# Performance work log

Hardware: AMD Instinct MI355X
Metric: run time of the kernel (lower is better)

The kernel has to match this reference:

```python
import jax, jax.numpy as jnp
import numpy as np


def setup_inputs() -> dict:
    key = jax.random.key(0)
    x = jax.random.normal(key, (4, 5, 256, 32, 32), dtype=jnp.float32)
    return {"x": x, "beta": 1}


def reference(x, beta):
    # x: [B, L, D, H, W] -> [B, L, H, W, D] -> [B, L, N, D], N = H*W
    B, L, D, H, W = x.shape
    xf = jnp.transpose(x, (0, 1, 3, 4, 2)).reshape(B, L, H * W, D)
    # scores: [B, L, N, N]
    scores = jnp.einsum('blnd,blmd->blnm', xf, xf)
    # exp(beta*s)/sum == softmax(beta*s) along last axis (numerically stable form)
    attention = jax.nn.softmax(beta * scores, axis=-1)
    # (x.unsqueeze(2) * attn.unsqueeze(4)).sum(3) == attn @ x
    return jnp.einsum('blnm,blmd->blnd', attention, xf)
```

## Files before the change

### kernel.cpp

```cpp
#include <hip/hip_runtime.h>


typedef __attribute__((ext_vector_type(8))) short bf16x8;
typedef __attribute__((ext_vector_type(4))) float f32x4;
typedef __attribute__((ext_vector_type(16))) float f32x16;

#define LDS_BARRIER() __asm__ volatile("s_waitcnt lgkmcnt(0)\ns_barrier" ::: "memory")

__device__ __forceinline__ unsigned int pack_bf16_rne(float a, float b) {
    unsigned int ua = __float_as_uint(a); ua += 0x7FFFu + ((ua >> 16) & 1u);
    unsigned int ub = __float_as_uint(b); ub += 0x7FFFu + ((ub >> 16) & 1u);
    return (ua >> 16) | (ub & 0xFFFF0000u);
}
__device__ __forceinline__ unsigned int pack2_trunc(float lo, float hi) {
    return __builtin_amdgcn_perm(__float_as_uint(hi), __float_as_uint(lo), 0x07060302u);
}

__global__ __launch_bounds__(256) void prep_kernel(const float* __restrict__ x,
                                                   unsigned short* __restrict__ XT,
                                                   unsigned short* __restrict__ XV) {
    __shared__ __align__(16) unsigned char smem[16384];
    int bid = blockIdx.x;
    int t = threadIdx.x;
    if (bid < 640) {
        uint4* T = (uint4*)smem;
        int slice = bid >> 5, w = bid & 31;
        int cc0 = (w & 3) * 32, d0 = (w >> 2) * 32;
        const float* xs = x + slice * 262144;
        int ccl = t & 31, dr = t >> 5;
        #pragma unroll
        for (int p = 0; p < 4; ++p) {
            int dl = p * 8 + dr;
            const float* src = xs + (d0 + dl) * 1024 + (cc0 + ccl) * 8;
            float4 a = *(const float4*)(src);
            float4 b = *(const float4*)(src + 4);
            uint4 o;
            o.x = pack_bf16_rne(a.x, a.y); o.y = pack_bf16_rne(a.z, a.w);
            o.z = pack_bf16_rne(b.x, b.y); o.w = pack_bf16_rne(b.z, b.w);
            T[ccl * 32 + (dl ^ ccl)] = o;
        }
        __syncthreads();
        unsigned short* xv = XV + slice * 262144;
        int dl2 = t & 31, cr = t >> 5;
        #pragma unroll
        for (int p = 0; p < 4; ++p) {
            int ccl2 = p * 8 + cr;
            uint4 o = T[ccl2 * 32 + (dl2 ^ ccl2)];
            *(uint4*)(xv + ((cc0 + ccl2) * 256 + d0 + dl2) * 8) = o;
        }
    } else {
        unsigned long long* TX = (unsigned long long*)smem;
        int b = bid - 640;
        int slice = b >> 5, w = b & 31;
        int d0 = (w & 1) * 128, n0 = (w >> 1) * 64;
        const float* xs = x + slice * 262144;
        int nq = t & 15, dqh = t >> 4;
        #pragma unroll
        for (int p = 0; p < 2; ++p) {
            int dq = p * 16 + dqh;
            const float* src = xs + (d0 + dq * 4) * 1024 + n0 + nq * 4;
            float4 r0 = *(const float4*)(src);
            float4 r1 = *(const float4*)(src + 1024);
            float4 r2 = *(const float4*)(src + 2048);
            float4 r3 = *(const float4*)(src + 3072);
            const float* f0 = (const float*)&r0; const float* f1 = (const float*)&r1;
            const float* f2 = (const float*)&r2; const float* f3 = (const float*)&r3;
            #pragma unroll
            for (int j = 0; j < 4; ++j) {
                int nl2 = nq * 4 + j;
                unsigned long long q = (unsigned long long)pack_bf16_rne(f0[j], f1[j])
                    | ((unsigned long long)pack_bf16_rne(f2[j], f3[j]) << 32);
                TX[nl2 * 32 + (dq ^ (nl2 & 31))] = q;
            }
        }
        __syncthreads();
        unsigned short* xt = XT + slice * 262144;
        int ch = t & 15, nr = t >> 4;
        #pragma unroll
        for (int p = 0; p < 4; ++p) {
            int nl2 = p * 16 + nr;
            unsigned long long qlo = TX[nl2 * 32 + ((ch * 2) ^ (nl2 & 31))];
            unsigned long long qhi = TX[nl2 * 32 + ((ch * 2 + 1) ^ (nl2 & 31))];
            uint4 o = make_uint4((unsigned int)qlo, (unsigned int)(qlo >> 32),
                                 (unsigned int)qhi, (unsigned int)(qhi >> 32));
            *(uint4*)(xt + (n0 + nl2) * 256 + ((((d0 >> 3) + ch) ^ (nl2 & 7)) * 8)) = o;
        }
    }
}

__global__ __launch_bounds__(256, 2) void attn_kernel(const unsigned short* __restrict__ XT,
                                                      const unsigned short* __restrict__ XV,
                                                      const int* __restrict__ beta,
                                                      float* __restrict__ out) {
    __shared__ __align__(16) unsigned short Pb[2][32 * 64];
    __shared__ float Lpart[4 * 32];
    __shared__ __align__(16) float Ltot[32];

    int bid = blockIdx.x;
    int t = ((bid & 7) * 80) + (bid >> 3);
    int slice = t >> 5, qh = t & 31;

    int tid = threadIdx.x;
    int lane = tid & 63, wv = tid >> 6;
    int nl = lane & 15, g = lane >> 4;
    int lo = lane & 31, hi = lane >> 5;

    const unsigned short* xt_s = XT + slice * 262144;
    const unsigned short* xv_s = XV + slice * 262144;
    float cscale = (float)(beta[0]) * 1.44269504089f;

    const unsigned short* kb = xt_s + (wv * 16 + nl) * 256;
    bf16x8 af[8];

    #pragma unroll
    for (int ks = 0; ks < 8; ++ks)
        af[ks] = *(const bf16x8*)(kb + (((ks * 4 + g) ^ (nl & 7)) * 8));

    bf16x8 qf[2][8];
    float mcol[2];
    #pragma unroll
    for (int nq = 0; nq < 2; ++nq) {
        int n = qh * 32 + nq * 16 + nl;
        const unsigned short* qrow = xt_s + n * 256;
        float dg = 0.f;
        #pragma unroll
        for (int ks = 0; ks < 8; ++ks) {
            qf[nq][ks] = *(const bf16x8*)(qrow + (((ks * 4 + g) ^ (n & 7)) * 8));
            const unsigned int* qu = (const unsigned int*)&qf[nq][ks];
            #pragma unroll
            for (int w = 0; w < 4; ++w) {
                float flo = __uint_as_float(qu[w] << 16);
                float fhi = __uint_as_float(qu[w] & 0xFFFF0000u);
                dg = fmaf(flo, flo, dg);
                dg = fmaf(fhi, fhi, dg);
            }
        }
        dg += __shfl_xor(dg, 16);
        dg += __shfl_xor(dg, 32);
        mcol[nq] = dg * cscale;
    }

    f32x16 acc[2];
    acc[0] = (f32x16)(0.f); acc[1] = (f32x16)(0.f);
    float lac0 = 0.f, lac1 = 0.f;

    const unsigned short* vb = xv_s + (hi * 256 + wv * 64 + lo) * 8;
    bf16x8 vf[8];
    #pragma unroll
    for (int ks = 0; ks < 4; ++ks) {
        vf[ks * 2]     = *(const bf16x8*)(vb + ks * 4096);
        vf[ks * 2 + 1] = *(const bf16x8*)(vb + ks * 4096 + 256);
    }

    for (int kt = 0; kt < 16; ++kt) {
        f32x4 s0 = {0.f,0.f,0.f,0.f}, s1 = {0.f,0.f,0.f,0.f};
        #pragma unroll
        for (int ks = 0; ks < 8; ++ks) {
            s0 = __builtin_amdgcn_mfma_f32_16x16x32_bf16(af[ks], qf[0][ks], s0, 0, 0, 0);
            s1 = __builtin_amdgcn_mfma_f32_16x16x32_bf16(af[ks], qf[1][ks], s1, 0, 0, 0);
        }

        if (kt < 15) {
            const unsigned short* kkt = kb + (kt + 1) * 16384;
            #pragma unroll
            for (int ks = 0; ks < 8; ++ks)
                af[ks] = *(const bf16x8*)(kkt + (((ks * 4 + g) ^ (nl & 7)) * 8));
        }

        {
            float p0 = exp2f(fmaf(s0[0], cscale, -mcol[0]));
            float p1 = exp2f(fmaf(s0[1], cscale, -mcol[0]));
            float p2 = exp2f(fmaf(s0[2], cscale, -mcol[0]));
            float p3 = exp2f(fmaf(s0[3], cscale, -mcol[0]));
            lac0 += (p0 + p1) + (p2 + p3);
            *(uint2*)(&Pb[kt & 1][nl * 64 + (((wv * 2 + (g >> 1)) ^ (nl & 7)) * 8) + (g & 1) * 4]) =
                make_uint2(pack2_trunc(p0, p1), pack2_trunc(p2, p3));
        }
        {
            float p0 = exp2f(fmaf(s1[0], cscale, -mcol[1]));
            float p1 = exp2f(fmaf(s1[1], cscale, -mcol[1]));
            float p2 = exp2f(fmaf(s1[2], cscale, -mcol[1]));
            float p3 = exp2f(fmaf(s1[3], cscale, -mcol[1]));
            lac1 += (p0 + p1) + (p2 + p3);
            *(uint2*)(&Pb[kt & 1][(16 + nl) * 64 + (((wv * 2 + (g >> 1)) ^ (nl & 7)) * 8) + (g & 1) * 4]) =
                make_uint2(pack2_trunc(p0, p1), pack2_trunc(p2, p3));
        }

        LDS_BARRIER();

        {
            const unsigned short* vnext = vb + (kt + 1) * 16384;
            #pragma unroll
            for (int ks = 0; ks < 4; ++ks) {
                bf16x8 pf = *(const bf16x8*)(&Pb[kt & 1][lo * 64 + (((ks * 2 + hi) ^ (lo & 7)) * 8)]);
                acc[0] = __builtin_amdgcn_mfma_f32_32x32x16_bf16(pf, vf[ks * 2],     acc[0], 0, 0, 0);
                acc[1] = __builtin_amdgcn_mfma_f32_32x32x16_bf16(pf, vf[ks * 2 + 1], acc[1], 0, 0, 0);
                if (kt < 15) {
                    vf[ks * 2]     = *(const bf16x8*)(vnext + ks * 4096);
                    vf[ks * 2 + 1] = *(const bf16x8*)(vnext + ks * 4096 + 256);
                }
            }
        }
    }

    lac0 += __shfl_xor(lac0, 16); lac0 += __shfl_xor(lac0, 32);
    lac1 += __shfl_xor(lac1, 16); lac1 += __shfl_xor(lac1, 32);
    if (lane < 16) {
        Lpart[wv * 32 + nl] = lac0;
        Lpart[wv * 32 + 16 + nl] = lac1;
    }
    LDS_BARRIER();
    if (tid < 32)
        Ltot[tid] = 1.f / (Lpart[tid] + Lpart[32 + tid] + Lpart[64 + tid] + Lpart[96 + tid]);
    LDS_BARRIER();

    float* outs = out + slice * 262144 + (qh * 32) * 256;
    #pragma unroll
    for (int rq = 0; rq < 4; ++rq) {
        f32x4 li = *(const f32x4*)(&Ltot[rq * 8 + hi * 4]);
        #pragma unroll
        for (int j = 0; j < 4; ++j) {
            int nloc = rq * 8 + hi * 4 + j;
            #pragma unroll
            for (int db = 0; db < 2; ++db)
                outs[nloc * 256 + wv * 64 + db * 32 + lo] = acc[db][rq * 4 + j] * li[j];
        }
    }
}

extern "C" void kernel_launch(void* const* d_in, const int* in_sizes, int n_in,
                              void* d_out, int out_size, void* d_ws, size_t ws_size,
                              hipStream_t stream) {
    const float* x = (const float*)d_in[0];
    const int* beta = (const int*)d_in[1];
    float* out = (float*)d_out;
    unsigned short* XT = (unsigned short*)d_ws;
    unsigned short* XV = (unsigned short*)d_ws + 5242880;
    prep_kernel<<<1280, 256, 0, stream>>>(x, XT, XV);
    attn_kernel<<<640, 256, 0, stream>>>(XT, XV, beta, out);
}
```

Before: 115.1 us.

## Process two key tiles per barrier with quad-buffered P staging

The main attention loop now handles two 64-key tiles per iteration. It writes both softmax probability tiles into a four-slot LDS buffer and then runs a single barrier before both PV MFMA passes, which halves the number of workgroup barriers. The extra LDS and longer live ranges may reduce occupancy or raise register pressure. The K and V fragment reloads stay serialized through the same register arrays, so the second PV must wait on a V reload.

Result: no change. 114.4 us (-0.6%).

```diff
diff --git a/kernel.cpp b/kernel.cpp
--- a/kernel.cpp
+++ b/kernel.cpp
@@ -92,7 +92,7 @@
                                                       const unsigned short* __restrict__ XV,
                                                       const int* __restrict__ beta,
                                                       float* __restrict__ out) {
-    __shared__ __align__(16) unsigned short Pb[2][32 * 64];
+    __shared__ __align__(16) unsigned short Pb[4][32 * 64];
     __shared__ float Lpart[4 * 32];
     __shared__ __align__(16) float Ltot[32];
 
@@ -152,28 +152,27 @@
         vf[ks * 2 + 1] = *(const bf16x8*)(vb + ks * 4096 + 256);
     }
 
-    for (int kt = 0; kt < 16; ++kt) {
-        f32x4 s0 = {0.f,0.f,0.f,0.f}, s1 = {0.f,0.f,0.f,0.f};
+    auto S_mfma = [&](f32x4& sx, f32x4& sy) {
         #pragma unroll
         for (int ks = 0; ks < 8; ++ks) {
-            s0 = __builtin_amdgcn_mfma_f32_16x16x32_bf16(af[ks], qf[0][ks], s0, 0, 0, 0);
-            s1 = __builtin_amdgcn_mfma_f32_16x16x32_bf16(af[ks], qf[1][ks], s1, 0, 0, 0);
-        }
-
-        if (kt < 15) {
-            const unsigned short* kkt = kb + (kt + 1) * 16384;
-            #pragma unroll
-            for (int ks = 0; ks < 8; ++ks)
-                af[ks] = *(const bf16x8*)(kkt + (((ks * 4 + g) ^ (nl & 7)) * 8));
-        }
-
+            sx = __builtin_amdgcn_mfma_f32_16x16x32_bf16(af[ks], qf[0][ks], sx, 0, 0, 0);
+            sy = __builtin_amdgcn_mfma_f32_16x16x32_bf16(af[ks], qf[1][ks], sy, 0, 0, 0);
+        }
+    };
+    auto issue_af = [&](int kt) {
+        const unsigned short* kkt = kb + kt * 16384;
+        #pragma unroll
+        for (int ks = 0; ks < 8; ++ks)
+            af[ks] = *(const bf16x8*)(kkt + (((ks * 4 + g) ^ (nl & 7)) * 8));
+    };
+    auto softmax_store = [&](const f32x4& s0, const f32x4& s1, int pbi) {
         {
             float p0 = exp2f(fmaf(s0[0], cscale, -mcol[0]));
             float p1 = exp2f(fmaf(s0[1], cscale, -mcol[0]));
             float p2 = exp2f(fmaf(s0[2], cscale, -mcol[0]));
             float p3 = exp2f(fmaf(s0[3], cscale, -mcol[0]));
             lac0 += (p0 + p1) + (p2 + p3);
-            *(uint2*)(&Pb[kt & 1][nl * 64 + (((wv * 2 + (g >> 1)) ^ (nl & 7)) * 8) + (g & 1) * 4]) =
+            *(uint2*)(&Pb[pbi][nl * 64 + (((wv * 2 + (g >> 1)) ^ (nl & 7)) * 8) + (g & 1) * 4]) =
                 make_uint2(pack2_trunc(p0, p1), pack2_trunc(p2, p3));
         }
         {
@@ -182,25 +181,42 @@
             float p2 = exp2f(fmaf(s1[2], cscale, -mcol[1]));
             float p3 = exp2f(fmaf(s1[3], cscale, -mcol[1]));
             lac1 += (p0 + p1) + (p2 + p3);
-            *(uint2*)(&Pb[kt & 1][(16 + nl) * 64 + (((wv * 2 + (g >> 1)) ^ (nl & 7)) * 8) + (g & 1) * 4]) =
+            *(uint2*)(&Pb[pbi][(16 + nl) * 64 + (((wv * 2 + (g >> 1)) ^ (nl & 7)) * 8) + (g & 1) * 4]) =
                 make_uint2(pack2_trunc(p0, p1), pack2_trunc(p2, p3));
         }
+    };
+    auto PV = [&](int pbi, bool reload, int ktn) {
+        const unsigned short* vnext = vb + ktn * 16384;
+        #pragma unroll
+        for (int ks = 0; ks < 4; ++ks) {
+            bf16x8 pf = *(const bf16x8*)(&Pb[pbi][lo * 64 + (((ks * 2 + hi) ^ (lo & 7)) * 8)]);
+            acc[0] = __builtin_amdgcn_mfma_f32_32x32x16_bf16(pf, vf[ks * 2],     acc[0], 0, 0, 0);
+            acc[1] = __builtin_amdgcn_mfma_f32_32x32x16_bf16(pf, vf[ks * 2 + 1], acc[1], 0, 0, 0);
+            if (reload) {
+                vf[ks * 2]     = *(const bf16x8*)(vnext + ks * 4096);
+                vf[ks * 2 + 1] = *(const bf16x8*)(vnext + ks * 4096 + 256);
+            }
+        }
+    };
+
+    for (int tt = 0; tt < 8; ++tt) {
+        int kt0 = tt * 2;
+        int pA = (tt & 1) * 2;
+
+        f32x4 s0 = {0.f,0.f,0.f,0.f}, s1 = {0.f,0.f,0.f,0.f};
+        S_mfma(s0, s1);
+        issue_af(kt0 + 1);
+        softmax_store(s0, s1, pA);
+
+        f32x4 s2 = {0.f,0.f,0.f,0.f}, s3 = {0.f,0.f,0.f,0.f};
+        S_mfma(s2, s3);
+        if (tt < 7) issue_af(kt0 + 2);
+        softmax_store(s2, s3, pA + 1);
 
         LDS_BARRIER();
 
-        {
-            const unsigned short* vnext = vb + (kt + 1) * 16384;
-            #pragma unroll
-            for (int ks = 0; ks < 4; ++ks) {
-                bf16x8 pf = *(const bf16x8*)(&Pb[kt & 1][lo * 64 + (((ks * 2 + hi) ^ (lo & 7)) * 8)]);
-                acc[0] = __builtin_amdgcn_mfma_f32_32x32x16_bf16(pf, vf[ks * 2],     acc[0], 0, 0, 0);
-                acc[1] = __builtin_amdgcn_mfma_f32_32x32x16_bf16(pf, vf[ks * 2 + 1], acc[1], 0, 0, 0);
-                if (kt < 15) {
-                    vf[ks * 2]     = *(const bf16x8*)(vnext + ks * 4096);
-                    vf[ks * 2 + 1] = *(const bf16x8*)(vnext + ks * 4096 + 256);
-                }
-            }
-        }
+        PV(pA, true, kt0 + 1);
+        PV(pA + 1, tt < 7, kt0 + 2);
     }
 
     lac0 += __shfl_xor(lac0, 16); lac0 += __shfl_xor(lac0, 32);
```

## Process two query tiles per block with 512-thread blocks sharing key/value streams

Applied to the files above, without the earlier changes.

Each block now holds 8 waves split into two halves, and each half handles its own 32-query tile, so a block covers 64 queries and the grid shrinks from 640 to 320 blocks. The two halves read the same key and value rows from global memory, which should improve L2/L1 reuse of K/V. Each half keeps separate P buffers and normalization sums. The cost is larger blocks, fewer of them (320 on a 256-CU part, a poor wave balance), and barriers that now synchronize 8 waves.

New measurement: 127.2 us. 1.1x slower.

```diff
diff --git a/kernel.cpp b/kernel.cpp
--- a/kernel.cpp
+++ b/kernel.cpp
@@ -88,20 +88,21 @@
     }
 }
 
-__global__ __launch_bounds__(256, 2) void attn_kernel(const unsigned short* __restrict__ XT,
+__global__ __launch_bounds__(512, 2) void attn_kernel(const unsigned short* __restrict__ XT,
                                                       const unsigned short* __restrict__ XV,
                                                       const int* __restrict__ beta,
                                                       float* __restrict__ out) {
-    __shared__ __align__(16) unsigned short Pb[2][32 * 64];
-    __shared__ float Lpart[4 * 32];
-    __shared__ __align__(16) float Ltot[32];
+    __shared__ __align__(16) unsigned short Pb[2][2][32 * 64];
+    __shared__ float Lpart[2 * 4 * 32];
+    __shared__ __align__(16) float Ltot[64];
 
     int bid = blockIdx.x;
-    int t = ((bid & 7) * 80) + (bid >> 3);
-    int slice = t >> 5, qh = t & 31;
+    int t = ((bid & 7) * 40) + (bid >> 3);
+    int slice = t >> 4, qh = t & 15;
 
     int tid = threadIdx.x;
     int lane = tid & 63, wv = tid >> 6;
+    int ms = wv & 3, h = wv >> 2;
     int nl = lane & 15, g = lane >> 4;
     int lo = lane & 31, hi = lane >> 5;
 
@@ -109,7 +110,7 @@
     const unsigned short* xv_s = XV + slice * 262144;
     float cscale = (float)(beta[0]) * 1.44269504089f;
 
-    const unsigned short* kb = xt_s + (wv * 16 + nl) * 256;
+    const unsigned short* kb = xt_s + (ms * 16 + nl) * 256;
     bf16x8 af[8];
 
     #pragma unroll
@@ -120,7 +121,7 @@
     float mcol[2];
     #pragma unroll
     for (int nq = 0; nq < 2; ++nq) {
-        int n = qh * 32 + nq * 16 + nl;
+        int n = qh * 64 + h * 32 + nq * 16 + nl;
         const unsigned short* qrow = xt_s + n * 256;
         float dg = 0.f;
         #pragma unroll
@@ -144,7 +145,7 @@
     acc[0] = (f32x16)(0.f); acc[1] = (f32x16)(0.f);
     float lac0 = 0.f, lac1 = 0.f;
 
-    const unsigned short* vb = xv_s + (hi * 256 + wv * 64 + lo) * 8;
+    const unsigned short* vb = xv_s + (hi * 256 + ms * 64 + lo) * 8;
     bf16x8 vf[8];
     #pragma unroll
     for (int ks = 0; ks < 4; ++ks) {
@@ -173,7 +174,7 @@
             float p2 = exp2f(fmaf(s0[2], cscale, -mcol[0]));
             float p3 = exp2f(fmaf(s0[3], cscale, -mcol[0]));
             lac0 += (p0 + p1) + (p2 + p3);
-            *(uint2*)(&Pb[kt & 1][nl * 64 + (((wv * 2 + (g >> 1)) ^ (nl & 7)) * 8) + (g & 1) * 4]) =
+            *(uint2*)(&Pb[kt & 1][h][nl * 64 + (((ms * 2 + (g >> 1)) ^ (nl & 7)) * 8) + (g & 1) * 4]) =
                 make_uint2(pack2_trunc(p0, p1), pack2_trunc(p2, p3));
         }
         {
@@ -182,7 +183,7 @@
             float p2 = exp2f(fmaf(s1[2], cscale, -mcol[1]));
             float p3 = exp2f(fmaf(s1[3], cscale, -mcol[1]));
             lac1 += (p0 + p1) + (p2 + p3);
-            *(uint2*)(&Pb[kt & 1][(16 + nl) * 64 + (((wv * 2 + (g >> 1)) ^ (nl & 7)) * 8) + (g & 1) * 4]) =
+            *(uint2*)(&Pb[kt & 1][h][(16 + nl) * 64 + (((ms * 2 + (g >> 1)) ^ (nl & 7)) * 8) + (g & 1) * 4]) =
                 make_uint2(pack2_trunc(p0, p1), pack2_trunc(p2, p3));
         }
 
@@ -192,7 +193,7 @@
             const unsigned short* vnext = vb + (kt + 1) * 16384;
             #pragma unroll
             for (int ks = 0; ks < 4; ++ks) {
-                bf16x8 pf = *(const bf16x8*)(&Pb[kt & 1][lo * 64 + (((ks * 2 + hi) ^ (lo & 7)) * 8)]);
+                bf16x8 pf = *(const bf16x8*)(&Pb[kt & 1][h][lo * 64 + (((ks * 2 + hi) ^ (lo & 7)) * 8)]);
                 acc[0] = __builtin_amdgcn_mfma_f32_32x32x16_bf16(pf, vf[ks * 2],     acc[0], 0, 0, 0);
                 acc[1] = __builtin_amdgcn_mfma_f32_32x32x16_bf16(pf, vf[ks * 2 + 1], acc[1], 0, 0, 0);
                 if (kt < 15) {
@@ -206,24 +207,27 @@
     lac0 += __shfl_xor(lac0, 16); lac0 += __shfl_xor(lac0, 32);
     lac1 += __shfl_xor(lac1, 16); lac1 += __shfl_xor(lac1, 32);
     if (lane < 16) {
-        Lpart[wv * 32 + nl] = lac0;
-        Lpart[wv * 32 + 16 + nl] = lac1;
+        Lpart[h * 128 + ms * 32 + nl] = lac0;
+        Lpart[h * 128 + ms * 32 + 16 + nl] = lac1;
     }
     LDS_BARRIER();
-    if (tid < 32)
-        Ltot[tid] = 1.f / (Lpart[tid] + Lpart[32 + tid] + Lpart[64 + tid] + Lpart[96 + tid]);
+    if (tid < 64) {
+        int hh = tid >> 5, r = tid & 31;
+        Ltot[tid] = 1.f / (Lpart[hh * 128 + r] + Lpart[hh * 128 + 32 + r] +
+                           Lpart[hh * 128 + 64 + r] + Lpart[hh * 128 + 96 + r]);
+    }
     LDS_BARRIER();
 
-    float* outs = out + slice * 262144 + (qh * 32) * 256;
+    float* outs = out + slice * 262144 + (qh * 64 + h * 32) * 256;
     #pragma unroll
     for (int rq = 0; rq < 4; ++rq) {
-        f32x4 li = *(const f32x4*)(&Ltot[rq * 8 + hi * 4]);
+        f32x4 li = *(const f32x4*)(&Ltot[h * 32 + rq * 8 + hi * 4]);
         #pragma unroll
         for (int j = 0; j < 4; ++j) {
             int nloc = rq * 8 + hi * 4 + j;
             #pragma unroll
             for (int db = 0; db < 2; ++db)
-                outs[nloc * 256 + wv * 64 + db * 32 + lo] = acc[db][rq * 4 + j] * li[j];
+                outs[nloc * 256 + ms * 64 + db * 32 + lo] = acc[db][rq * 4 + j] * li[j];
         }
     }
 }
@@ -237,5 +241,5 @@
     unsigned short* XT = (unsigned short*)d_ws;
     unsigned short* XV = (unsigned short*)d_ws + 5242880;
     prep_kernel<<<1280, 256, 0, stream>>>(x, XT, XV);
-    attn_kernel<<<640, 256, 0, stream>>>(XT, XV, beta, out);
-}
+    attn_kernel<<<320, 512, 0, stream>>>(XT, XV, beta, out);
+}
```
